# Optimization experiments

Measured on AMD Instinct MI355X. Metric: run time of the kernel, lower is better.

## Reference

```python
import jax, jax.numpy as jnp
import numpy as np

B, S = 1, 4096
H, KV, D, HID = 8, 4, 256, 2304   # heads, kv heads, head_dim, hidden_size
G = H // KV                        # GQA group size
WINDOW = 1024                      # sliding window
THETA = 10000.0                    # rope_local_base_freq (sliding attention)
EPS = 1e-6
SCALE = 256.0 ** -0.5              # query_pre_attn_scalar ** -0.5


def rms_norm(x, w, eps=EPS):
    # Gemma3RMSNorm: fp32 rms over last dim, scale by (1 + weight)
    v = jnp.mean(jnp.square(x), axis=-1, keepdims=True)
    return x * jax.lax.rsqrt(v + eps) * (1.0 + w)


def rope(x, position_ids):
    # x: [B, S, N, D]; split-half rotation as in Gemma3RotaryEmbedding
    d = x.shape[-1]
    inv_freq = 1.0 / (THETA ** (jnp.arange(0, d, 2, dtype=jnp.float32) / d))  # [D/2]
    freqs = position_ids.astype(jnp.float32)[:, :, None] * inv_freq  # [B, S, D/2]
    cos = jnp.cos(freqs)[:, :, None, :]  # [B, S, 1, D/2]
    sin = jnp.sin(freqs)[:, :, None, :]
    x1, x2 = jnp.split(x, 2, axis=-1)
    return jnp.concatenate([x1 * cos - x2 * sin, x1 * sin + x2 * cos], axis=-1)


def setup_inputs() -> dict:
    key = jax.random.key(0)
    ks = jax.random.split(key, 6)
    n = lambda k, shp, sc: jax.random.normal(k, shp, dtype=jnp.float32) * sc
    return {
        "x": n(ks[0], (B, S, HID), 1.0),
        "position_ids": jnp.broadcast_to(jnp.arange(S, dtype=jnp.int32)[None, :], (B, S)),
        "wq": n(ks[1], (HID, H * D), 0.02),
        "wk": n(ks[2], (HID, KV * D), 0.02),
        "wv": n(ks[3], (HID, KV * D), 0.02),
        "wo": n(ks[4], (H * D, HID), 0.02),
        "q_norm_w": jnp.zeros((D,), dtype=jnp.float32),
        "k_norm_w": jnp.zeros((D,), dtype=jnp.float32),
    }


def reference(x, position_ids, wq, wk, wv, wo, q_norm_w, k_norm_w):
    b, s, _ = x.shape
    q = (x @ wq).reshape(b, s, H, D)
    k = (x @ wk).reshape(b, s, KV, D)
    v = (x @ wv).reshape(b, s, KV, D)

    # QK-RMSNorm over head_dim, then RoPE, then query scaling
    q = rms_norm(q, q_norm_w)
    k = rms_norm(k, k_norm_w)
    q = rope(q, position_ids)
    k = rope(k, position_ids)
    q = q * SCALE

    # GQA: group queries over shared KV heads. qg: [B, S, KV, G, D]
    qg = q.reshape(b, s, KV, G, D)
    scores = jnp.einsum('bqcgd,btcd->bcgqt', qg, k)  # [B, KV, G, S, S]

    # causal + sliding-window mask: t <= q and q - t < WINDOW
    pi = position_ids[:, :, None]  # query positions [B, S, 1]
    pj = position_ids[:, None, :]  # key positions   [B, 1, S]
    mask = (pj <= pi) & (pi - pj < WINDOW)  # [B, S, S]
    neg = jnp.finfo(scores.dtype).min
    scores = jnp.where(mask[:, None, None, :, :], scores, neg)

    probs = jax.nn.softmax(scores, axis=-1)
    out = jnp.einsum('bcgqt,btcd->bqcgd', probs, v).reshape(b, s, H * D)
    return out @ wo
```

## Files before the change

### kernel.cpp

```cpp
#include <hip/hip_runtime.h>
#include <stdint.h>

typedef unsigned short u16;
typedef __attribute__((ext_vector_type(8))) short bf16x8;
typedef __attribute__((ext_vector_type(4))) float f32x4;

#define S_LEN 4096
#define HID_DIM 2304
#define QKV_N 4096
#define AO_N 2048
#define HD 256
#define WIN 1024
#define QSCALE 0.0625f

static __device__ __forceinline__ u16 f2bf(float f) {
  union { float f; uint32_t u; } v; v.f = f;
  return (u16)((v.u + 0x7FFFu + ((v.u >> 16) & 1u)) >> 16);
}
static __device__ __forceinline__ float bf2f(u16 h) {
  union { uint32_t u; float f; } v; v.u = ((uint32_t)h) << 16;
  return v.f;
}

static __device__ __forceinline__ void gld16(const void* src, void* dst) {
  __builtin_amdgcn_global_load_lds((const __attribute__((address_space(1))) void*)src,
                                   (__attribute__((address_space(3))) void*)dst, 16, 0, 0);
}

#define BAR() __builtin_amdgcn_s_barrier()
#define LG0() asm volatile("s_waitcnt lgkmcnt(0)" ::: "memory")
#define VM4() asm volatile("s_waitcnt vmcnt(4)" ::: "memory")
#define VM2() asm volatile("s_waitcnt vmcnt(2)" ::: "memory")
#define VM0() asm volatile("s_waitcnt vmcnt(0)" ::: "memory")
#define PRIO1() __builtin_amdgcn_s_setprio(1)
#define PRIO0() __builtin_amdgcn_s_setprio(0)

__global__ __launch_bounds__(256) void k_cvt_bf16(const float* __restrict__ in,
                                                  u16* __restrict__ out, int n) {
  int i = (blockIdx.x * 256 + threadIdx.x) * 4;
  if (i >= n) return;
  float4 v = *(const float4*)(in + i);
  uint64_t p = (uint64_t)f2bf(v.x) | ((uint64_t)f2bf(v.y) << 16)
             | ((uint64_t)f2bf(v.z) << 32) | ((uint64_t)f2bf(v.w) << 48);
  *(uint64_t*)(out + i) = p;
}

__global__ __launch_bounds__(256) void k_transpose_cvt(const float* __restrict__ in, int C,
                                                       u16* __restrict__ out, int out_stride,
                                                       int row_off) {
  __shared__ float tile[32][33];
  int c0 = blockIdx.x * 32, r0 = blockIdx.y * 32;
  int tx = threadIdx.x & 31, ty = threadIdx.x >> 5;
#pragma unroll
  for (int i = 0; i < 4; i++)
    tile[ty + i * 8][tx] = in[(size_t)(r0 + ty + i * 8) * C + c0 + tx];
  __syncthreads();
#pragma unroll
  for (int i = 0; i < 4; i++)
    out[(size_t)(row_off + c0 + ty + i * 8) * out_stride + r0 + tx] = f2bf(tile[tx][ty + i * 8]);
}

__global__ __launch_bounds__(256) void k_transpose_w(const float* __restrict__ wq,
                                                     const float* __restrict__ wk,
                                                     const float* __restrict__ wv,
                                                     u16* __restrict__ out) {
  int ct = blockIdx.x;
  int r0 = blockIdx.y * 32;
  const float* src;
  int C, c0;
  if (ct < 64) {
    src = wq; C = 2048; c0 = ct * 32;
  } else if (ct < 96) {
    src = wk; C = 1024; c0 = (ct - 64) * 32;
  } else {
    src = wv; C = 1024; c0 = (ct - 96) * 32;
  }
  __shared__ float tile[32][33];
  int tx = threadIdx.x & 31, ty = threadIdx.x >> 5;
#pragma unroll
  for (int i = 0; i < 4; i++)
    tile[ty + i * 8][tx] = src[(size_t)(r0 + ty + i * 8) * C + c0 + tx];
  __syncthreads();
#pragma unroll
  for (int i = 0; i < 4; i++)
    out[(size_t)(ct * 32 + ty + i * 8) * HID_DIM + r0 + tx] = f2bf(tile[tx][ty + i * 8]);
}

__global__ __launch_bounds__(256) void k_vtrans(const u16* __restrict__ qkv,
                                                u16* __restrict__ vtout) {
  __shared__ u16 tile[32][33];
  int c0 = blockIdx.x * 32, s0 = blockIdx.y * 32;
  int tx = threadIdx.x & 31, ty = threadIdx.x >> 5;
#pragma unroll
  for (int i = 0; i < 4; i++)
    tile[ty + i * 8][tx] = qkv[(size_t)(s0 + ty + i * 8) * QKV_N + 3072 + c0 + tx];
  __syncthreads();
#pragma unroll
  for (int i = 0; i < 4; i++)
    vtout[(size_t)(c0 + ty + i * 8) * S_LEN + s0 + tx] = tile[tx][ty + i * 8];
}

template <int OUT_BF16>
__global__ __launch_bounds__(512, 2) void k_gemm8p(const u16* __restrict__ A,
                                                   const u16* __restrict__ Bt,
                                                   void* __restrict__ Cout,
                                                   int M, int N, int K) {
  __shared__ u16 sA[2][256 * 64];
  __shared__ u16 sB[2][256 * 64];
  const int t = threadIdx.x, lane = t & 63, wave = t >> 6;
  const int wr = wave >> 2, wc = wave & 3;
  const int l15 = lane & 15, l4 = lane >> 4;
  const int nbn = N >> 8;
  const int cpx = gridDim.x >> 3;
  const int wg = ((int)blockIdx.x & 7) * cpx + ((int)blockIdx.x >> 3);
  const int bm = wg / nbn, bn = wg % nbn;
  const int NT = K >> 6;
  const int srow = lane >> 3;
  const int sslot = ((lane & 7) ^ srow) * 8;
  const u16* Abase = A + (size_t)(bm * 256) * K;
  const u16* Bbase = Bt + (size_t)(bn * 256) * K;
  f32x4 acc[8][4] = {};
  bf16x8 aF[4][2], b01[2][2], b23[2][2];

#define STG_A(BUF, HALF, KT) do {                                                 \
    _Pragma("unroll")                                                             \
    for (int c_ = 0; c_ < 2; c_++) {                                              \
      int rb_ = (HALF) * 128 + (wave * 2 + c_) * 8;                               \
      gld16(Abase + (size_t)(rb_ + srow) * K + ((KT) << 6) + sslot,               \
            &sA[BUF][rb_ * 64]);                                                  \
    }                                                                             \
  } while (0)
#define STG_B(BUF, HALF, KT) do {                                                 \
    _Pragma("unroll")                                                             \
    for (int c_ = 0; c_ < 2; c_++) {                                              \
      int rb_ = (HALF) * 128 + (wave * 2 + c_) * 8;                               \
      gld16(Bbase + (size_t)(rb_ + srow) * K + ((KT) << 6) + sslot,               \
            &sB[BUF][rb_ * 64]);                                                  \
    }                                                                             \
  } while (0)
#define LDA(BUF, M_, KK)                                                          \
  (*(const bf16x8*)&sA[BUF][((M_) * 32 + wr * 16 + l15) * 64 +                    \
                            ((((KK) << 2) + l4) ^ (l15 & 7)) * 8])
#define LDB(BUF, N_, KK)                                                          \
  (*(const bf16x8*)&sB[BUF][((N_) * 64 + wc * 16 + l15) * 64 +                    \
                            ((((KK) << 2) + l4) ^ (l15 & 7)) * 8])

#define P1_LOADS(b_) do {                                                         \
    _Pragma("unroll") for (int m_ = 0; m_ < 4; m_++)                              \
      _Pragma("unroll") for (int k_ = 0; k_ < 2; k_++)                            \
        aF[m_][k_] = LDA(b_, m_, k_);                                             \
    _Pragma("unroll") for (int n_ = 0; n_ < 2; n_++)                              \
      _Pragma("unroll") for (int k_ = 0; k_ < 2; k_++)                            \
        b01[n_][k_] = LDB(b_, n_, k_);                                            \
  } while (0)
#define P2_LOADS(b_) do {                                                         \
    _Pragma("unroll") for (int n_ = 0; n_ < 2; n_++)                              \
      _Pragma("unroll") for (int k_ = 0; k_ < 2; k_++)                            \
        b23[n_][k_] = LDB(b_, n_ + 2, k_);                                        \
  } while (0)
#define P3_LOADS(b_) do {                                                         \
    _Pragma("unroll") for (int m_ = 0; m_ < 4; m_++)                              \
      _Pragma("unroll") for (int k_ = 0; k_ < 2; k_++)                            \
        aF[m_][k_] = LDA(b_, m_ + 4, k_);                                         \
  } while (0)
#define MFMA16(MOFF, NOFF, BREG) do {                                             \
    _Pragma("unroll") for (int m_ = 0; m_ < 4; m_++)                              \
      _Pragma("unroll") for (int n_ = 0; n_ < 2; n_++)                            \
        _Pragma("unroll") for (int k_ = 0; k_ < 2; k_++)                          \
          acc[m_ + MOFF][n_ + NOFF] = __builtin_amdgcn_mfma_f32_16x16x32_bf16(    \
              aF[m_][k_], BREG[n_][k_], acc[m_ + MOFF][n_ + NOFF], 0, 0, 0);      \
  } while (0)

  STG_A(0, 0, 0);
  STG_B(0, 0, 0);
  STG_B(0, 1, 0);
  STG_A(0, 1, 0);
  VM4();
  BAR();

  for (int tt = 0; tt < NT - 1; ++tt) {
    const int b = tt & 1, nb = b ^ 1;
    P1_LOADS(b);
    STG_A(nb, 0, tt + 1);
    BAR(); LG0(); PRIO1(); MFMA16(0, 0, b01); PRIO0();
    VM4();
    BAR();
    P2_LOADS(b);
    STG_B(nb, 0, tt + 1);
    BAR(); LG0(); PRIO1(); MFMA16(0, 2, b23); PRIO0();
    VM4();
    BAR();
    P3_LOADS(b);
    STG_B(nb, 1, tt + 1);
    BAR(); LG0(); PRIO1(); MFMA16(4, 0, b01); PRIO0();
    BAR();
    STG_A(nb, 1, tt + 1);
    BAR(); PRIO1(); MFMA16(4, 2, b23); PRIO0();
    VM4();
    BAR();
  }
  {
    const int b = (NT - 1) & 1;
    P1_LOADS(b);
    BAR(); LG0(); PRIO1(); MFMA16(0, 0, b01); PRIO0();
    VM2();
    BAR();
    P2_LOADS(b);
    BAR(); LG0(); PRIO1(); MFMA16(0, 2, b23); PRIO0();
    VM0();
    BAR();
    P3_LOADS(b);
    BAR(); LG0(); PRIO1(); MFMA16(4, 0, b01); PRIO0();
    BAR();
    PRIO1(); MFMA16(4, 2, b23); PRIO0();
  }

#pragma unroll
  for (int m = 0; m < 8; m++)
#pragma unroll
    for (int n = 0; n < 4; n++)
#pragma unroll
      for (int r = 0; r < 4; r++) {
        size_t row = bm * 256 + m * 32 + wr * 16 + l4 * 4 + r;
        size_t col = bn * 256 + n * 64 + wc * 16 + l15;
        if (OUT_BF16)
          ((u16*)Cout)[row * N + col] = f2bf(acc[m][n][r]);
        else
          ((float*)Cout)[row * N + col] = acc[m][n][r];
      }
#undef STG_A
#undef STG_B
#undef LDA
#undef LDB
#undef P1_LOADS
#undef P2_LOADS
#undef P3_LOADS
#undef MFMA16
}

__global__ __launch_bounds__(128) void k_normrope(u16* __restrict__ qkv,
                                                  const int* __restrict__ pos_ids,
                                                  const float* __restrict__ qw,
                                                  const float* __restrict__ kw) {
  __shared__ float cross[2];
  int idx = blockIdx.x;
  int s = idx / 12, r = idx % 12;
  bool is_q = (r < 8);
  u16* p = qkv + (size_t)s * QKV_N + (is_q ? r * HD : 2048 + (r - 8) * HD);
  const float* w = is_q ? qw : kw;
  int j = threadIdx.x;
  float x1 = bf2f(p[j]), x2 = bf2f(p[j + 128]);
  float ss = x1 * x1 + x2 * x2;
#pragma unroll
  for (int off = 1; off < 64; off <<= 1) ss += __shfl_xor(ss, off);
  if ((threadIdx.x & 63) == 0) cross[threadIdx.x >> 6] = ss;
  __syncthreads();
  float rms = rsqrtf((cross[0] + cross[1]) * (1.0f / 256.0f) + 1e-6f);
  float y1 = x1 * rms * (1.0f + w[j]);
  float y2 = x2 * rms * (1.0f + w[j + 128]);
  float ang = (float)pos_ids[s] * exp2f((float)j * (-13.287712379549449f / 128.0f));
  float sn, c;
  sincosf(ang, &sn, &c);
  float sc = is_q ? QSCALE : 1.0f;
  p[j] = f2bf((y1 * c - y2 * sn) * sc);
  p[j + 128] = f2bf((y1 * sn + y2 * c) * sc);
}

__global__ __launch_bounds__(512, 2) void k_attn(const u16* __restrict__ qkv,
                                                 const u16* __restrict__ vt,
                                                 const int* __restrict__ pos_ids,
                                                 u16* __restrict__ aout) {
  __shared__ u16 lK[64 * 256];
  __shared__ u16 lV[256 * 64];
  __shared__ u16 lP[8][16 * 64];
  const int bid = blockIdx.x;
  const int wg = (bid & 7) * 32 + (bid >> 3);
  const int kvh = wg >> 6;
  const int q0 = (wg & 63) * 64;
  const int t = threadIdx.x, lane = t & 63, wave = t >> 6;
  const int l15 = lane & 15, l4 = lane >> 4;
  const int head = kvh * 2 + (wave >> 2);
  const int qw = q0 + (wave & 3) * 16;

  bf16x8 qfr[8];
  {
    const u16* qptr = qkv + (size_t)(qw + l15) * QKV_N + head * HD + l4 * 8;
#pragma unroll
    for (int kc = 0; kc < 8; kc++) qfr[kc] = *(const bf16x8*)(qptr + kc * 32);
  }
  f32x4 acc[16] = {};
  float mrow[4], lrow[4];
#pragma unroll
  for (int r = 0; r < 4; r++) { mrow[r] = -1e30f; lrow[r] = 0.0f; }
  int qi[4];
#pragma unroll
  for (int r = 0; r < 4; r++) qi[r] = pos_ids[qw + l4 * 4 + r];

  const int krw = lane >> 5, kcl = lane & 31;
  const int vrw = lane >> 3, vcl = lane & 7;
  const u16* kgb = qkv + 2048 + kvh * HD;
  const u16* vgb = vt + (size_t)kvh * HD * S_LEN;

  int start = q0 - (WIN - 1);
  if (start < 0) start = 0;
  start &= ~63;

#define STAGE_KV(T0) do {                                                             \
    _Pragma("unroll")                                                                 \
    for (int i_ = 0; i_ < 4; i_++) {                                                  \
      int ch_ = wave * 4 + i_;                                                        \
      int kr_ = ch_ * 2 + krw;                                                        \
      gld16(kgb + (size_t)((T0) + kr_) * QKV_N + ((kcl ^ (kr_ & 7)) * 8),             \
            &lK[ch_ * 512]);                                                          \
      int vr_ = ch_ * 8 + vrw;                                                        \
      gld16(vgb + (size_t)vr_ * S_LEN + (T0) + ((vcl ^ (vr_ & 7)) * 8),               \
            &lV[ch_ * 512]);                                                          \
    }                                                                                 \
  } while (0)

  for (int t0 = start; t0 <= q0 + 63; t0 += 64) {
    STAGE_KV(t0);
    int kp[4];
#pragma unroll
    for (int kb = 0; kb < 4; kb++) kp[kb] = pos_ids[t0 + kb * 16 + l15];
    __syncthreads();
    f32x4 sv[4] = {};
    PRIO1();
#pragma unroll
    for (int kb = 0; kb < 4; kb++) {
      const char* krow = (const char*)&lK[(kb * 16 + l15) * 256];
      const int sw = ((kb * 16 + l15) & 7) << 4;
#pragma unroll
      for (int kc = 0; kc < 8; kc++) {
        bf16x8 kf = *(const bf16x8*)(krow + ((kc * 64 + l4 * 16) ^ sw));
        sv[kb] = __builtin_amdgcn_mfma_f32_16x16x32_bf16(qfr[kc], kf, sv[kb], 0, 0, 0);
      }
    }
    PRIO0();
    float sloc[4][4], mx[4];
    float need = 0.0f;
#pragma unroll
    for (int r = 0; r < 4; r++) {
      int pi = qi[r];
#pragma unroll
      for (int kb = 0; kb < 4; kb++)
        sloc[r][kb] = ((kp[kb] <= pi) && (pi - kp[kb] < WIN)) ? sv[kb][r] : -__builtin_inff();
      float m_ = fmaxf(fmaxf(sloc[r][0], sloc[r][1]), fmaxf(sloc[r][2], sloc[r][3]));
#pragma unroll
      for (int off = 1; off < 16; off <<= 1) m_ = fmaxf(m_, __shfl_xor(m_, off));
      mx[r] = m_;
      need = fmaxf(need, m_ - mrow[r]);
    }
    bool resc = __any(need > 8.0f);
    if (resc) {
#pragma unroll
      for (int r = 0; r < 4; r++) {
        float nm = fmaxf(mrow[r], mx[r]);
        float al = __expf(mrow[r] - nm);
        mrow[r] = nm;
        lrow[r] *= al;
#pragma unroll
        for (int nd = 0; nd < 16; nd++) acc[nd][r] *= al;
      }
    }
#pragma unroll
    for (int r = 0; r < 4; r++) {
      float nm = mrow[r];
      float e0 = __expf(sloc[r][0] - nm), e1 = __expf(sloc[r][1] - nm);
      float e2 = __expf(sloc[r][2] - nm), e3 = __expf(sloc[r][3] - nm);
      float sum = (e0 + e1) + (e2 + e3);
#pragma unroll
      for (int off = 1; off < 16; off <<= 1) sum += __shfl_xor(sum, off);
      lrow[r] += sum;
      int q = l4 * 4 + r;
      char* lpw = (char*)&lP[wave][0] + q * 128;
      int swp = (q & 7) << 4;
      *(u16*)(lpw + ((l15 * 2) ^ swp)) = f2bf(e0);
      *(u16*)(lpw + ((32 + l15 * 2) ^ swp)) = f2bf(e1);
      *(u16*)(lpw + ((64 + l15 * 2) ^ swp)) = f2bf(e2);
      *(u16*)(lpw + ((96 + l15 * 2) ^ swp)) = f2bf(e3);
    }
#pragma unroll
    for (int kc2 = 0; kc2 < 2; kc2++) {
      int q = l15;
      bf16x8 pa = *(const bf16x8*)((const char*)&lP[wave][0] + q * 128 +
                                   ((kc2 * 64 + l4 * 16) ^ ((q & 7) << 4)));
      PRIO1();
#pragma unroll
      for (int nd = 0; nd < 16; nd++) {
        int d = nd * 16 + l15;
        bf16x8 vf = *(const bf16x8*)((const char*)&lV[d * 64] +
                                     ((kc2 * 64 + l4 * 16) ^ ((d & 7) << 4)));
        acc[nd] = __builtin_amdgcn_mfma_f32_16x16x32_bf16(pa, vf, acc[nd], 0, 0, 0);
      }
      PRIO0();
    }
    __syncthreads();
  }
  float rinv[4];
#pragma unroll
  for (int r = 0; r < 4; r++) rinv[r] = 1.0f / lrow[r];
#pragma unroll
  for (int nd = 0; nd < 16; nd++)
#pragma unroll
    for (int r = 0; r < 4; r++) {
      size_t row = qw + l4 * 4 + r;
      aout[row * AO_N + head * HD + nd * 16 + l15] = f2bf(acc[nd][r] * rinv[r]);
    }
#undef STAGE_KV
}

extern "C" void kernel_launch(void* const* d_in, const int* in_sizes, int n_in,
                              void* d_out, int out_size, void* d_ws, size_t ws_size,
                              hipStream_t stream) {
  const float* x = (const float*)d_in[0];
  const int* pos = (const int*)d_in[1];
  const float* wq = (const float*)d_in[2];
  const float* wk = (const float*)d_in[3];
  const float* wv = (const float*)d_in[4];
  const float* wo = (const float*)d_in[5];
  const float* qnw = (const float*)d_in[6];
  const float* knw = (const float*)d_in[7];

  u16* qkv = (u16*)d_out;
  u16* xbf = (u16*)d_ws;
  u16* wT = (u16*)((char*)d_ws + 18874368);
  u16* vtb = (u16*)((char*)d_ws + 28311552);
  u16* aout = xbf;

  k_cvt_bf16<<<9216, 256, 0, stream>>>(x, xbf, S_LEN * HID_DIM);
  k_transpose_w<<<dim3(128, 72), 256, 0, stream>>>(wq, wk, wv, wT);
  k_gemm8p<1><<<dim3(256), 512, 0, stream>>>(xbf, wT, qkv, S_LEN, QKV_N, HID_DIM);
  k_vtrans<<<dim3(32, 128), 256, 0, stream>>>(qkv, vtb);
  k_normrope<<<S_LEN * 12, 128, 0, stream>>>(qkv, pos, qnw, knw);
  k_transpose_cvt<<<dim3(72, 64), 256, 0, stream>>>(wo, HID_DIM, wT, 2048, 0);
  k_attn<<<dim3(256), 512, 0, stream>>>(qkv, vtb, pos, aout);
  k_gemm8p<0><<<dim3(144), 512, 0, stream>>>(aout, wT, d_out, S_LEN, HID_DIM, 2048);
}
```

Baseline: 266.1 us.

## Use 256x192 tile GEMM for output projection to fill more CUs

Adds a new GEMM kernel with 256x192 output tiles and a four-phase pipelined LDS double-buffer schedule, used for the final attention-output by wo projection. With N=2304 the old 256x256 tiling gave 144 workgroups. The 192-wide tiling gives 192 workgroups, which spreads better over the GPU's compute units. The cost is lower per-tile arithmetic intensity and a different barrier/waitcnt schedule that has to be correct.

```diff
diff --git a/kernel.cpp b/kernel.cpp
--- a/kernel.cpp
+++ b/kernel.cpp
@@ -30,6 +30,7 @@
 #define BAR() __builtin_amdgcn_s_barrier()
 #define LG0() asm volatile("s_waitcnt lgkmcnt(0)" ::: "memory")
 #define VM4() asm volatile("s_waitcnt vmcnt(4)" ::: "memory")
+#define VM3() asm volatile("s_waitcnt vmcnt(3)" ::: "memory")
 #define VM2() asm volatile("s_waitcnt vmcnt(2)" ::: "memory")
 #define VM0() asm volatile("s_waitcnt vmcnt(0)" ::: "memory")
 #define PRIO1() __builtin_amdgcn_s_setprio(1)
@@ -238,6 +239,144 @@
 #undef MFMA16
 }
 
+__global__ __launch_bounds__(512, 2) void k_gemm192(const u16* __restrict__ A,
+                                                    const u16* __restrict__ Bt,
+                                                    float* __restrict__ Cout,
+                                                    int M, int N, int K) {
+  __shared__ u16 sA[2][256 * 64];
+  __shared__ u16 sB[2][192 * 64];
+  const int t = threadIdx.x, lane = t & 63, wave = t >> 6;
+  const int wr = wave >> 2, wc = wave & 3;
+  const int l15 = lane & 15, l4 = lane >> 4;
+  const int nbn = N / 192;
+  const int cpx = gridDim.x >> 3;
+  const int wg = ((int)blockIdx.x & 7) * cpx + ((int)blockIdx.x >> 3);
+  const int bm = wg / nbn, bn = wg % nbn;
+  const int NT = K >> 6;
+  const int srow = lane >> 3;
+  const int sslot = ((lane & 7) ^ srow) * 8;
+  const u16* Abase = A + (size_t)(bm * 256) * K;
+  const u16* Bbase = Bt + (size_t)(bn * 192) * K;
+  f32x4 acc[8][3] = {};
+  bf16x8 aF[4][2], b01[2][2], b2[2];
+
+#define GA_STG_A(BUF, HALF, KT) do {                                              \
+    _Pragma("unroll")                                                             \
+    for (int c_ = 0; c_ < 2; c_++) {                                              \
+      int rb_ = (HALF) * 128 + (wave * 2 + c_) * 8;                               \
+      gld16(Abase + (size_t)(rb_ + srow) * K + ((KT) << 6) + sslot,               \
+            &sA[BUF][rb_ * 64]);                                                  \
+    }                                                                             \
+  } while (0)
+#define GA_STG_BC(BUF, CH, KT) do {                                               \
+    int rb_ = (CH) * 64 + wave * 8;                                               \
+    gld16(Bbase + (size_t)(rb_ + srow) * K + ((KT) << 6) + sslot,                 \
+          &sB[BUF][rb_ * 64]);                                                    \
+  } while (0)
+#define GA_LDA(BUF, M_, KK)                                                       \
+  (*(const bf16x8*)&sA[BUF][((M_) * 32 + wr * 16 + l15) * 64 +                    \
+                            ((((KK) << 2) + l4) ^ (l15 & 7)) * 8])
+#define GA_LDB(BUF, N_, KK)                                                       \
+  (*(const bf16x8*)&sB[BUF][((N_) * 64 + wc * 16 + l15) * 64 +                    \
+                            ((((KK) << 2) + l4) ^ (l15 & 7)) * 8])
+#define GA_P1_LOADS(b_) do {                                                      \
+    _Pragma("unroll") for (int m_ = 0; m_ < 4; m_++)                              \
+      _Pragma("unroll") for (int k_ = 0; k_ < 2; k_++)                            \
+        aF[m_][k_] = GA_LDA(b_, m_, k_);                                          \
+    _Pragma("unroll") for (int n_ = 0; n_ < 2; n_++)                              \
+      _Pragma("unroll") for (int k_ = 0; k_ < 2; k_++)                            \
+        b01[n_][k_] = GA_LDB(b_, n_, k_);                                         \
+  } while (0)
+#define GA_P2_LOADS(b_) do {                                                      \
+    _Pragma("unroll") for (int k_ = 0; k_ < 2; k_++)                              \
+      b2[k_] = GA_LDB(b_, 2, k_);                                                 \
+  } while (0)
+#define GA_P3_LOADS(b_) do {                                                      \
+    _Pragma("unroll") for (int m_ = 0; m_ < 4; m_++)                              \
+      _Pragma("unroll") for (int k_ = 0; k_ < 2; k_++)                            \
+        aF[m_][k_] = GA_LDA(b_, m_ + 4, k_);                                      \
+  } while (0)
+#define GA_MFMA_N01(MOFF) do {                                                    \
+    _Pragma("unroll") for (int m_ = 0; m_ < 4; m_++)                              \
+      _Pragma("unroll") for (int n_ = 0; n_ < 2; n_++)                            \
+        _Pragma("unroll") for (int k_ = 0; k_ < 2; k_++)                          \
+          acc[m_ + MOFF][n_] = __builtin_amdgcn_mfma_f32_16x16x32_bf16(           \
+              aF[m_][k_], b01[n_][k_], acc[m_ + MOFF][n_], 0, 0, 0);              \
+  } while (0)
+#define GA_MFMA_N2(MOFF) do {                                                     \
+    _Pragma("unroll") for (int m_ = 0; m_ < 4; m_++)                              \
+      _Pragma("unroll") for (int k_ = 0; k_ < 2; k_++)                            \
+        acc[m_ + MOFF][2] = __builtin_amdgcn_mfma_f32_16x16x32_bf16(              \
+            aF[m_][k_], b2[k_], acc[m_ + MOFF][2], 0, 0, 0);                      \
+  } while (0)
+
+  GA_STG_A(0, 0, 0);
+  GA_STG_BC(0, 0, 0);
+  GA_STG_BC(0, 1, 0);
+  GA_STG_BC(0, 2, 0);
+  GA_STG_A(0, 1, 0);
+  VM3();
+  BAR();
+
+  for (int tt = 0; tt < NT - 1; ++tt) {
+    const int b = tt & 1, nb = b ^ 1;
+    GA_P1_LOADS(b);
+    GA_STG_A(nb, 0, tt + 1);
+    BAR(); LG0(); PRIO1(); GA_MFMA_N01(0); PRIO0();
+    VM4();
+    BAR();
+    GA_P2_LOADS(b);
+    GA_STG_BC(nb, 0, tt + 1);
+    GA_STG_BC(nb, 1, tt + 1);
+    BAR(); LG0(); PRIO1(); GA_MFMA_N2(0); PRIO0();
+    VM4();
+    BAR();
+    GA_P3_LOADS(b);
+    GA_STG_BC(nb, 2, tt + 1);
+    BAR(); LG0(); PRIO1(); GA_MFMA_N01(4); PRIO0();
+    BAR();
+    GA_STG_A(nb, 1, tt + 1);
+    BAR(); PRIO1(); GA_MFMA_N2(4); PRIO0();
+    VM3();
+    BAR();
+  }
+  {
+    const int b = (NT - 1) & 1;
+    GA_P1_LOADS(b);
+    BAR(); LG0(); PRIO1(); GA_MFMA_N01(0); PRIO0();
+    VM2();
+    BAR();
+    GA_P2_LOADS(b);
+    BAR(); LG0(); PRIO1(); GA_MFMA_N2(0); PRIO0();
+    VM0();
+    BAR();
+    GA_P3_LOADS(b);
+    BAR(); LG0(); PRIO1(); GA_MFMA_N01(4); PRIO0();
+    BAR();
+    PRIO1(); GA_MFMA_N2(4); PRIO0();
+  }
+
+#pragma unroll
+  for (int m = 0; m < 8; m++)
+#pragma unroll
+    for (int n = 0; n < 3; n++)
+#pragma unroll
+      for (int r = 0; r < 4; r++) {
+        size_t row = bm * 256 + m * 32 + wr * 16 + l4 * 4 + r;
+        size_t col = bn * 192 + n * 64 + wc * 16 + l15;
+        Cout[row * N + col] = acc[m][n][r];
+      }
+#undef GA_STG_A
+#undef GA_STG_BC
+#undef GA_LDA
+#undef GA_LDB
+#undef GA_P1_LOADS
+#undef GA_P2_LOADS
+#undef GA_P3_LOADS
+#undef GA_MFMA_N01
+#undef GA_MFMA_N2
+}
+
 __global__ __launch_bounds__(128) void k_normrope(u16* __restrict__ qkv,
                                                   const int* __restrict__ pos_ids,
                                                   const float* __restrict__ qw,
@@ -435,5 +574,5 @@
   k_normrope<<<S_LEN * 12, 128, 0, stream>>>(qkv, pos, qnw, knw);
   k_transpose_cvt<<<dim3(72, 64), 256, 0, stream>>>(wo, HID_DIM, wT, 2048, 0);
   k_attn<<<dim3(256), 512, 0, stream>>>(qkv, vtb, pos, aout);
-  k_gemm8p<0><<<dim3(144), 512, 0, stream>>>(aout, wT, d_out, S_LEN, HID_DIM, 2048);
-}
+  k_gemm192<<<dim3(192), 512, 0, stream>>>(aout, wT, (float*)d_out, S_LEN, HID_DIM, 2048);
+}
```

Result: faster. 260.3 us (-2.2%).
